# Optimization experiments

Measured on AMD Instinct MI355X. Metric: run time of the kernel, lower is better.

## Reference

```python
import jax, jax.numpy as jnp
import numpy as np

N_NODES = 100000
FEAT_DIM = 128
EMBED_DIM = 128
NUM_SAMPLE = 10


def setup_inputs() -> dict:
    key = jax.random.key(0)
    k1, k2, k3, k4, k5 = jax.random.split(key, 5)
    features = jax.random.normal(k1, (N_NODES, FEAT_DIM), dtype=jnp.float32)
    W1 = jax.random.normal(k2, (EMBED_DIM, FEAT_DIM), dtype=jnp.float32) * (1.0 / np.sqrt(FEAT_DIM))
    W2 = jax.random.normal(k3, (EMBED_DIM, EMBED_DIM), dtype=jnp.float32) * (1.0 / np.sqrt(EMBED_DIM))
    adj = jax.random.randint(k4, (N_NODES, NUM_SAMPLE), 0, N_NODES, dtype=jnp.int64)
    nodes = jax.random.randint(k5, (N_NODES,), 0, N_NODES, dtype=jnp.int64)
    return {"features": features, "W1": W1, "W2": W2, "adj": adj, "nodes": nodes}


def reference(features, W1, W2, adj, nodes):
    # 2-layer GraphSAGE with gcn=True: mean over {self} U sampled neighbors,
    # then relu(agg @ W.T). Layer 1 is computed for all nodes since layer 2
    # needs embeddings of arbitrary neighbors.
    n = features.shape[0]
    self_idx = jnp.arange(n, dtype=adj.dtype)[:, None]            # [N,1]
    neigh1 = jnp.concatenate([self_idx, adj], axis=1)             # [N,S+1]
    agg1 = jnp.mean(features[neigh1], axis=1)                     # [N,F] (gather+mean)
    h1 = jax.nn.relu(agg1 @ W1.T)                                 # [N,E]

    neigh2 = jnp.concatenate([nodes[:, None], adj[nodes]], axis=1)  # [B,S+1]
    agg2 = jnp.mean(h1[neigh2], axis=1)                           # [B,E]
    out = jax.nn.relu(agg2 @ W2.T).T                              # [E,B], Encoder returns embed_dim x num_nodes
    return out
```

## Files before the change

### kernel.cpp

```cpp
#include <hip/hip_runtime.h>

#define N_NODES 100000
#define DIM 128
#define NS 10
#define SCALE (1.0f / 11.0f)
#define NE2 ((size_t)N_NODES * 64)

typedef unsigned int uint;
typedef unsigned short ushort;
typedef __attribute__((ext_vector_type(8))) short bf16x8;
typedef __attribute__((ext_vector_type(4))) float f32x4;

__device__ inline float bl(uint u) {
    union { uint x; float f; } c; c.x = u << 16; return c.f;
}
__device__ inline uint f2b(float x) {
    union { float f; uint u; } c; c.f = x;
    return (c.u + 0x7FFFu + ((c.u >> 16) & 1u)) >> 16;
}

__global__ __launch_bounds__(256) void wsplit(const float* __restrict__ W1,
                                              const float* __restrict__ W2,
                                              ushort* __restrict__ o) {
    const int i = blockIdx.x * 256 + threadIdx.x;
    const float a = W1[i];
    uint h = f2b(a);
    o[i] = (ushort)h;
    o[16384 + i] = (ushort)f2b(a - bl(h));
    const float b = W2[i];
    h = f2b(b);
    o[32768 + i] = (ushort)h;
    o[49152 + i] = (ushort)f2b(b - bl(h));
}

__global__ __launch_bounds__(256, 2) void gemm1(const float* __restrict__ X,
                                                const ushort* __restrict__ Whi,
                                                const ushort* __restrict__ Wlo,
                                                ushort* __restrict__ C) {
    __shared__ __align__(16) ushort lds[8192];
    const int t = threadIdx.x;
    const int lane = t & 63;
    const int wave = t >> 6;
    const int m16 = lane & 15;
    const int kq = lane >> 4;
    const int r0 = blockIdx.x * 32;

    const int v0 = t, v1 = t + 256;
    const int ln0 = v0 & 63, ln1 = v1 & 63;
    const float* s0 = X + (size_t)(r0 + (v0 >> 8) * 16 + (ln0 & 15)) * DIM +
                      ((v0 >> 6) & 3) * 32 + (ln0 >> 4) * 8;
    const float* s1 = X + (size_t)(r0 + (v1 >> 8) * 16 + (ln1 & 15)) * DIM +
                      ((v1 >> 6) & 3) * 32 + (ln1 >> 4) * 8;
    const float4 f00 = *(const float4*)(s0);
    const float4 f01 = *(const float4*)(s0 + 4);
    const float4 f10 = *(const float4*)(s1);
    const float4 f11 = *(const float4*)(s1 + 4);

    bf16x8 wh[2][4], wl[2][4];
#pragma unroll
    for (int c = 0; c < 2; ++c)
#pragma unroll
        for (int ks = 0; ks < 4; ++ks) {
            const size_t off = (size_t)((2 * wave + c) * 16 + m16) * DIM + ks * 32 + kq * 8;
            wh[c][ks] = *(const bf16x8*)(Whi + off);
            wl[c][ks] = *(const bf16x8*)(Wlo + off);
        }

    {
        const float xs[8] = {f00.x, f00.y, f00.z, f00.w, f01.x, f01.y, f01.z, f01.w};
        bf16x8 hi, lo;
#pragma unroll
        for (int j = 0; j < 8; ++j) {
            const uint hb = f2b(xs[j]);
            hi[j] = (short)hb;
            lo[j] = (short)f2b(xs[j] - bl(hb));
        }
        *(bf16x8*)(lds + (v0 >> 6) * 512 + ln0 * 8) = hi;
        *(bf16x8*)(lds + 4096 + (v0 >> 6) * 512 + ln0 * 8) = lo;
    }
    {
        const float xs[8] = {f10.x, f10.y, f10.z, f10.w, f11.x, f11.y, f11.z, f11.w};
        bf16x8 hi, lo;
#pragma unroll
        for (int j = 0; j < 8; ++j) {
            const uint hb = f2b(xs[j]);
            hi[j] = (short)hb;
            lo[j] = (short)f2b(xs[j] - bl(hb));
        }
        *(bf16x8*)(lds + (v1 >> 6) * 512 + ln1 * 8) = hi;
        *(bf16x8*)(lds + 4096 + (v1 >> 6) * 512 + ln1 * 8) = lo;
    }
    __syncthreads();

    f32x4 acc[2][2];
#pragma unroll
    for (int bt = 0; bt < 2; ++bt)
#pragma unroll
        for (int c = 0; c < 2; ++c) acc[bt][c] = (f32x4){0.f, 0.f, 0.f, 0.f};

#pragma unroll
    for (int ks = 0; ks < 4; ++ks) {
#pragma unroll
        for (int bt = 0; bt < 2; ++bt) {
            const int g = bt * 4 + ks;
            const bf16x8 xh = *(const bf16x8*)(lds + g * 512 + lane * 8);
            const bf16x8 xl = *(const bf16x8*)(lds + 4096 + g * 512 + lane * 8);
#pragma unroll
            for (int c = 0; c < 2; ++c) {
                acc[bt][c] = __builtin_amdgcn_mfma_f32_16x16x32_bf16(wh[c][ks], xh, acc[bt][c], 0, 0, 0);
                acc[bt][c] = __builtin_amdgcn_mfma_f32_16x16x32_bf16(wl[c][ks], xh, acc[bt][c], 0, 0, 0);
                acc[bt][c] = __builtin_amdgcn_mfma_f32_16x16x32_bf16(wh[c][ks], xl, acc[bt][c], 0, 0, 0);
            }
        }
    }

#pragma unroll
    for (int bt = 0; bt < 2; ++bt) {
        const size_t row = (size_t)(r0 + bt * 16 + m16);
#pragma unroll
        for (int c = 0; c < 2; ++c) {
            uint2 w;
            w.x = f2b(acc[bt][c][0]) | (f2b(acc[bt][c][1]) << 16);
            w.y = f2b(acc[bt][c][2]) | (f2b(acc[bt][c][3]) << 16);
            *(uint2*)(C + (size_t)(wave >> 1) * NE2 + row * 64 +
                      (2 * (wave & 1) + c) * 16 + kq * 4) = w;
        }
    }
}

__global__ __launch_bounds__(256) void agg1(const ushort* __restrict__ FW,
                                            const int* __restrict__ adj,
                                            ushort* __restrict__ H) {
    __shared__ int idx_lds[320];
    const int t = threadIdx.x;
    const int r0 = blockIdx.x * 32;
    for (int l = t; l < 320; l += 256)
        idx_lds[l] = adj[(size_t)r0 * NS + l];
    __syncthreads();
    const int team = t >> 4;
    const int j = t & 15;
    const int ri0 = team * 2, ri1 = team * 2 + 1;
#pragma unroll
    for (int p = 0; p < 2; ++p) {
        const ushort* FWp = FW + (size_t)p * NE2;
        ushort* Hp = H + (size_t)p * NE2;
        uint2 u0[11], u1[11];
        u0[0] = ((const uint2*)(FWp + (size_t)(r0 + ri0) * 64))[j];
#pragma unroll
        for (int s = 0; s < NS; ++s)
            u0[1 + s] = ((const uint2*)(FWp + (size_t)idx_lds[ri0 * NS + s] * 64))[j];
        u1[0] = ((const uint2*)(FWp + (size_t)(r0 + ri1) * 64))[j];
#pragma unroll
        for (int s = 0; s < NS; ++s)
            u1[1 + s] = ((const uint2*)(FWp + (size_t)idx_lds[ri1 * NS + s] * 64))[j];
        float a0 = 0.f, a1 = 0.f, a2 = 0.f, a3 = 0.f;
        float b0 = 0.f, b1 = 0.f, b2 = 0.f, b3 = 0.f;
#pragma unroll
        for (int s = 0; s < 11; ++s) {
            a0 += bl(u0[s].x); a1 += bl(u0[s].x >> 16);
            a2 += bl(u0[s].y); a3 += bl(u0[s].y >> 16);
            b0 += bl(u1[s].x); b1 += bl(u1[s].x >> 16);
            b2 += bl(u1[s].y); b3 += bl(u1[s].y >> 16);
        }
        uint2 w;
        w.x = f2b(fmaxf(a0 * SCALE, 0.f)) | (f2b(fmaxf(a1 * SCALE, 0.f)) << 16);
        w.y = f2b(fmaxf(a2 * SCALE, 0.f)) | (f2b(fmaxf(a3 * SCALE, 0.f)) << 16);
        ((uint2*)(Hp + (size_t)(r0 + ri0) * 64))[j] = w;
        w.x = f2b(fmaxf(b0 * SCALE, 0.f)) | (f2b(fmaxf(b1 * SCALE, 0.f)) << 16);
        w.y = f2b(fmaxf(b2 * SCALE, 0.f)) | (f2b(fmaxf(b3 * SCALE, 0.f)) << 16);
        ((uint2*)(Hp + (size_t)(r0 + ri1) * 64))[j] = w;
    }
}

__global__ __launch_bounds__(256) void agg2b(const ushort* __restrict__ H,
                                             const int* __restrict__ adj,
                                             const int* __restrict__ nodes,
                                             ushort* __restrict__ P) {
    __shared__ int idx_lds[32 * 11];
    const int t = threadIdx.x;
    const int r0 = blockIdx.x * 32;
    if (t < 32) idx_lds[t * 11] = nodes[r0 + t];
    __syncthreads();
    for (int l = t; l < 320; l += 256) {
        const int bi = l / 10;
        const int s = l - bi * 10;
        idx_lds[bi * 11 + 1 + s] = adj[(size_t)idx_lds[bi * 11] * NS + s];
    }
    __syncthreads();
    const int team = t >> 4;
    const int j = t & 15;
    const int ri0 = team * 2, ri1 = team * 2 + 1;
#pragma unroll
    for (int p = 0; p < 2; ++p) {
        const ushort* Hp = H + (size_t)p * NE2;
        ushort* Pp = P + (size_t)p * NE2;
        uint2 u0[11], u1[11];
#pragma unroll
        for (int s = 0; s < 11; ++s)
            u0[s] = ((const uint2*)(Hp + (size_t)idx_lds[ri0 * 11 + s] * 64))[j];
#pragma unroll
        for (int s = 0; s < 11; ++s)
            u1[s] = ((const uint2*)(Hp + (size_t)idx_lds[ri1 * 11 + s] * 64))[j];
        float a0 = 0.f, a1 = 0.f, a2 = 0.f, a3 = 0.f;
        float b0 = 0.f, b1 = 0.f, b2 = 0.f, b3 = 0.f;
#pragma unroll
        for (int s = 0; s < 11; ++s) {
            a0 += bl(u0[s].x); a1 += bl(u0[s].x >> 16);
            a2 += bl(u0[s].y); a3 += bl(u0[s].y >> 16);
            b0 += bl(u1[s].x); b1 += bl(u1[s].x >> 16);
            b2 += bl(u1[s].y); b3 += bl(u1[s].y >> 16);
        }
        uint2 w;
        w.x = f2b(a0 * SCALE) | (f2b(a1 * SCALE) << 16);
        w.y = f2b(a2 * SCALE) | (f2b(a3 * SCALE) << 16);
        ((uint2*)(Pp + (size_t)(r0 + ri0) * 64))[j] = w;
        w.x = f2b(b0 * SCALE) | (f2b(b1 * SCALE) << 16);
        w.y = f2b(b2 * SCALE) | (f2b(b3 * SCALE) << 16);
        ((uint2*)(Pp + (size_t)(r0 + ri1) * 64))[j] = w;
    }
}

__global__ __launch_bounds__(256, 2) void gemm2t(const ushort* __restrict__ P,
                                                 const ushort* __restrict__ Whi,
                                                 const ushort* __restrict__ Wlo,
                                                 float* __restrict__ out) {
    __shared__ __align__(16) ushort lds[4096];
    const int t = threadIdx.x;
    const int lane = t & 63;
    const int wave = t >> 6;
    const int m16 = lane & 15;
    const int kq = lane >> 4;
    const int r0 = blockIdx.x * 32;

    const int v0 = t, v1 = t + 256;
    const int ln0 = v0 & 63, ln1 = v1 & 63;
    const int ksq0 = (v0 >> 6) & 3, ksq1 = (v1 >> 6) & 3;
    const ushort* s0 = P + (size_t)(ksq0 >> 1) * NE2 +
                       (size_t)(r0 + (v0 >> 8) * 16 + (ln0 & 15)) * 64 +
                       (ksq0 & 1) * 32 + (ln0 >> 4) * 8;
    const ushort* s1 = P + (size_t)(ksq1 >> 1) * NE2 +
                       (size_t)(r0 + (v1 >> 8) * 16 + (ln1 & 15)) * 64 +
                       (ksq1 & 1) * 32 + (ln1 >> 4) * 8;
    const bf16x8 p0 = *(const bf16x8*)(s0);
    const bf16x8 p1 = *(const bf16x8*)(s1);

    bf16x8 wh[2][4], wl[2][4];
#pragma unroll
    for (int c = 0; c < 2; ++c)
#pragma unroll
        for (int ks = 0; ks < 4; ++ks) {
            const size_t off = (size_t)((2 * wave + c) * 16 + m16) * DIM + ks * 32 + kq * 8;
            wh[c][ks] = *(const bf16x8*)(Whi + off);
            wl[c][ks] = *(const bf16x8*)(Wlo + off);
        }

    *(bf16x8*)(lds + (v0 >> 6) * 512 + ln0 * 8) = p0;
    *(bf16x8*)(lds + (v1 >> 6) * 512 + ln1 * 8) = p1;
    __syncthreads();

    f32x4 acc[2][2];
#pragma unroll
    for (int bt = 0; bt < 2; ++bt)
#pragma unroll
        for (int c = 0; c < 2; ++c) acc[bt][c] = (f32x4){0.f, 0.f, 0.f, 0.f};

#pragma unroll
    for (int ks = 0; ks < 4; ++ks) {
#pragma unroll
        for (int bt = 0; bt < 2; ++bt) {
            const bf16x8 pa = *(const bf16x8*)(lds + (bt * 4 + ks) * 512 + lane * 8);
#pragma unroll
            for (int c = 0; c < 2; ++c) {
                acc[bt][c] = __builtin_amdgcn_mfma_f32_16x16x32_bf16(pa, wh[c][ks], acc[bt][c], 0, 0, 0);
                acc[bt][c] = __builtin_amdgcn_mfma_f32_16x16x32_bf16(pa, wl[c][ks], acc[bt][c], 0, 0, 0);
            }
        }
    }

#pragma unroll
    for (int bt = 0; bt < 2; ++bt) {
        const int b = r0 + bt * 16 + kq * 4;
#pragma unroll
        for (int c = 0; c < 2; ++c) {
            const int e = (2 * wave + c) * 16 + m16;
            float4 v;
            v.x = fmaxf(acc[bt][c][0], 0.f);
            v.y = fmaxf(acc[bt][c][1], 0.f);
            v.z = fmaxf(acc[bt][c][2], 0.f);
            v.w = fmaxf(acc[bt][c][3], 0.f);
            *(float4*)(out + (size_t)e * N_NODES + b) = v;
        }
    }
}

extern "C" void kernel_launch(void* const* d_in, const int* in_sizes, int n_in,
                              void* d_out, int out_size, void* d_ws, size_t ws_size,
                              hipStream_t stream) {
    const float* features = (const float*)d_in[0];
    const float* W1 = (const float*)d_in[1];
    const float* W2 = (const float*)d_in[2];
    const int* adj = (const int*)d_in[3];
    const int* nodes = (const int*)d_in[4];
    float* out = (float*)d_out;

    const size_t NE = (size_t)N_NODES * DIM;
    ushort* fw = (ushort*)d_ws;
    ushort* h1 = fw + NE;
    ushort* wpl = h1 + NE;
    ushort* w1hi = wpl;
    ushort* w1lo = wpl + 16384;
    ushort* w2hi = wpl + 32768;
    ushort* w2lo = wpl + 49152;

    wsplit<<<64, 256, 0, stream>>>(W1, W2, wpl);
    gemm1<<<N_NODES / 32, 256, 0, stream>>>(features, w1hi, w1lo, fw);
    agg1<<<N_NODES / 32, 256, 0, stream>>>(fw, adj, h1);
    agg2b<<<N_NODES / 32, 256, 0, stream>>>(h1, adj, nodes, fw);
    gemm2t<<<N_NODES / 32, 256, 0, stream>>>(fw, w2hi, w2lo, out);
}
```

Measured before the change: 154.7 us.

## Fuse layer-2 neighbor aggregation into the layer-2 MFMA GEMM kernel

Merges the agg2b gather-mean kernel and the gemm2t GEMM kernel into one 512-thread kernel. Each thread gathers 11 neighbor rows as 16-byte loads, averages them, and writes the bf16 result straight into LDS in MFMA operand layout. This removes the global round trip of the aggregated matrix and one kernel launch. The cost is larger blocks with more registers per thread, and each wave now handles one 16-column output slice instead of two.

```diff
diff --git a/kernel.cpp b/kernel.cpp
--- a/kernel.cpp
+++ b/kernel.cpp
@@ -172,59 +172,14 @@
     }
 }
 
-__global__ __launch_bounds__(256) void agg2b(const ushort* __restrict__ H,
-                                             const int* __restrict__ adj,
-                                             const int* __restrict__ nodes,
-                                             ushort* __restrict__ P) {
+__global__ __launch_bounds__(512) void gemm2f2(const ushort* __restrict__ H,
+                                               const int* __restrict__ adj,
+                                               const int* __restrict__ nodes,
+                                               const ushort* __restrict__ Whi,
+                                               const ushort* __restrict__ Wlo,
+                                               float* __restrict__ out) {
+    __shared__ __align__(16) ushort plds[4096];
     __shared__ int idx_lds[32 * 11];
-    const int t = threadIdx.x;
-    const int r0 = blockIdx.x * 32;
-    if (t < 32) idx_lds[t * 11] = nodes[r0 + t];
-    __syncthreads();
-    for (int l = t; l < 320; l += 256) {
-        const int bi = l / 10;
-        const int s = l - bi * 10;
-        idx_lds[bi * 11 + 1 + s] = adj[(size_t)idx_lds[bi * 11] * NS + s];
-    }
-    __syncthreads();
-    const int team = t >> 4;
-    const int j = t & 15;
-    const int ri0 = team * 2, ri1 = team * 2 + 1;
-#pragma unroll
-    for (int p = 0; p < 2; ++p) {
-        const ushort* Hp = H + (size_t)p * NE2;
-        ushort* Pp = P + (size_t)p * NE2;
-        uint2 u0[11], u1[11];
-#pragma unroll
-        for (int s = 0; s < 11; ++s)
-            u0[s] = ((const uint2*)(Hp + (size_t)idx_lds[ri0 * 11 + s] * 64))[j];
-#pragma unroll
-        for (int s = 0; s < 11; ++s)
-            u1[s] = ((const uint2*)(Hp + (size_t)idx_lds[ri1 * 11 + s] * 64))[j];
-        float a0 = 0.f, a1 = 0.f, a2 = 0.f, a3 = 0.f;
-        float b0 = 0.f, b1 = 0.f, b2 = 0.f, b3 = 0.f;
-#pragma unroll
-        for (int s = 0; s < 11; ++s) {
-            a0 += bl(u0[s].x); a1 += bl(u0[s].x >> 16);
-            a2 += bl(u0[s].y); a3 += bl(u0[s].y >> 16);
-            b0 += bl(u1[s].x); b1 += bl(u1[s].x >> 16);
-            b2 += bl(u1[s].y); b3 += bl(u1[s].y >> 16);
-        }
-        uint2 w;
-        w.x = f2b(a0 * SCALE) | (f2b(a1 * SCALE) << 16);
-        w.y = f2b(a2 * SCALE) | (f2b(a3 * SCALE) << 16);
-        ((uint2*)(Pp + (size_t)(r0 + ri0) * 64))[j] = w;
-        w.x = f2b(b0 * SCALE) | (f2b(b1 * SCALE) << 16);
-        w.y = f2b(b2 * SCALE) | (f2b(b3 * SCALE) << 16);
-        ((uint2*)(Pp + (size_t)(r0 + ri1) * 64))[j] = w;
-    }
-}
-
-__global__ __launch_bounds__(256, 2) void gemm2t(const ushort* __restrict__ P,
-                                                 const ushort* __restrict__ Whi,
-                                                 const ushort* __restrict__ Wlo,
-                                                 float* __restrict__ out) {
-    __shared__ __align__(16) ushort lds[4096];
     const int t = threadIdx.x;
     const int lane = t & 63;
     const int wave = t >> 6;
@@ -232,64 +187,69 @@
     const int kq = lane >> 4;
     const int r0 = blockIdx.x * 32;
 
-    const int v0 = t, v1 = t + 256;
-    const int ln0 = v0 & 63, ln1 = v1 & 63;
-    const int ksq0 = (v0 >> 6) & 3, ksq1 = (v1 >> 6) & 3;
-    const ushort* s0 = P + (size_t)(ksq0 >> 1) * NE2 +
-                       (size_t)(r0 + (v0 >> 8) * 16 + (ln0 & 15)) * 64 +
-                       (ksq0 & 1) * 32 + (ln0 >> 4) * 8;
-    const ushort* s1 = P + (size_t)(ksq1 >> 1) * NE2 +
-                       (size_t)(r0 + (v1 >> 8) * 16 + (ln1 & 15)) * 64 +
-                       (ksq1 & 1) * 32 + (ln1 >> 4) * 8;
-    const bf16x8 p0 = *(const bf16x8*)(s0);
-    const bf16x8 p1 = *(const bf16x8*)(s1);
-
-    bf16x8 wh[2][4], wl[2][4];
-#pragma unroll
-    for (int c = 0; c < 2; ++c)
-#pragma unroll
-        for (int ks = 0; ks < 4; ++ks) {
-            const size_t off = (size_t)((2 * wave + c) * 16 + m16) * DIM + ks * 32 + kq * 8;
-            wh[c][ks] = *(const bf16x8*)(Whi + off);
-            wl[c][ks] = *(const bf16x8*)(Wlo + off);
-        }
-
-    *(bf16x8*)(lds + (v0 >> 6) * 512 + ln0 * 8) = p0;
-    *(bf16x8*)(lds + (v1 >> 6) * 512 + ln1 * 8) = p1;
-    __syncthreads();
-
-    f32x4 acc[2][2];
-#pragma unroll
-    for (int bt = 0; bt < 2; ++bt)
-#pragma unroll
-        for (int c = 0; c < 2; ++c) acc[bt][c] = (f32x4){0.f, 0.f, 0.f, 0.f};
-
+    bf16x8 wh[4], wl[4];
 #pragma unroll
     for (int ks = 0; ks < 4; ++ks) {
+        const size_t off = (size_t)(wave * 16 + m16) * DIM + ks * 32 + kq * 8;
+        wh[ks] = *(const bf16x8*)(Whi + off);
+        wl[ks] = *(const bf16x8*)(Wlo + off);
+    }
+
+    if (t < 32) idx_lds[t * 11] = nodes[r0 + t];
+    __syncthreads();
+    if (t < 320) {
+        const int bi = t / 10;
+        const int s = t - bi * 10;
+        idx_lds[bi * 11 + 1 + s] = adj[(size_t)idx_lds[bi * 11] * NS + s];
+    }
+    __syncthreads();
+
+    const int ri = (t >> 8) * 16 + (t & 15);
+    const int k0 = ((t >> 6) & 3) * 32 + ((t >> 4) & 3) * 8;
+    const ushort* Hp = H + (size_t)(k0 >> 6) * NE2 + (k0 & 63);
+    uint4 u[11];
+#pragma unroll
+    for (int s = 0; s < 11; ++s)
+        u[s] = *(const uint4*)(Hp + (size_t)idx_lds[ri * 11 + s] * 64);
+    float a[8];
+#pragma unroll
+    for (int k = 0; k < 8; ++k) a[k] = 0.f;
+#pragma unroll
+    for (int s = 0; s < 11; ++s) {
+        a[0] += bl(u[s].x); a[1] += bl(u[s].x >> 16);
+        a[2] += bl(u[s].y); a[3] += bl(u[s].y >> 16);
+        a[4] += bl(u[s].z); a[5] += bl(u[s].z >> 16);
+        a[6] += bl(u[s].w); a[7] += bl(u[s].w >> 16);
+    }
+    bf16x8 pw;
+#pragma unroll
+    for (int k = 0; k < 8; ++k) pw[k] = (short)f2b(a[k] * SCALE);
+    *(bf16x8*)(plds + t * 8) = pw;
+    __syncthreads();
+
+    f32x4 acc[2];
+    acc[0] = (f32x4){0.f, 0.f, 0.f, 0.f};
+    acc[1] = (f32x4){0.f, 0.f, 0.f, 0.f};
+#pragma unroll
+    for (int ks = 0; ks < 4; ++ks) {
 #pragma unroll
         for (int bt = 0; bt < 2; ++bt) {
-            const bf16x8 pa = *(const bf16x8*)(lds + (bt * 4 + ks) * 512 + lane * 8);
-#pragma unroll
-            for (int c = 0; c < 2; ++c) {
-                acc[bt][c] = __builtin_amdgcn_mfma_f32_16x16x32_bf16(pa, wh[c][ks], acc[bt][c], 0, 0, 0);
-                acc[bt][c] = __builtin_amdgcn_mfma_f32_16x16x32_bf16(pa, wl[c][ks], acc[bt][c], 0, 0, 0);
-            }
-        }
-    }
-
+            const bf16x8 pa = *(const bf16x8*)(plds + (bt * 4 + ks) * 512 + lane * 8);
+            acc[bt] = __builtin_amdgcn_mfma_f32_16x16x32_bf16(pa, wh[ks], acc[bt], 0, 0, 0);
+            acc[bt] = __builtin_amdgcn_mfma_f32_16x16x32_bf16(pa, wl[ks], acc[bt], 0, 0, 0);
+        }
+    }
+
+    const int e = wave * 16 + m16;
 #pragma unroll
     for (int bt = 0; bt < 2; ++bt) {
         const int b = r0 + bt * 16 + kq * 4;
-#pragma unroll
-        for (int c = 0; c < 2; ++c) {
-            const int e = (2 * wave + c) * 16 + m16;
-            float4 v;
-            v.x = fmaxf(acc[bt][c][0], 0.f);
-            v.y = fmaxf(acc[bt][c][1], 0.f);
-            v.z = fmaxf(acc[bt][c][2], 0.f);
-            v.w = fmaxf(acc[bt][c][3], 0.f);
-            *(float4*)(out + (size_t)e * N_NODES + b) = v;
-        }
+        float4 v;
+        v.x = fmaxf(acc[bt][0], 0.f);
+        v.y = fmaxf(acc[bt][1], 0.f);
+        v.z = fmaxf(acc[bt][2], 0.f);
+        v.w = fmaxf(acc[bt][3], 0.f);
+        *(float4*)(out + (size_t)e * N_NODES + b) = v;
     }
 }
 
@@ -315,6 +275,5 @@
     wsplit<<<64, 256, 0, stream>>>(W1, W2, wpl);
     gemm1<<<N_NODES / 32, 256, 0, stream>>>(features, w1hi, w1lo, fw);
     agg1<<<N_NODES / 32, 256, 0, stream>>>(fw, adj, h1);
-    agg2b<<<N_NODES / 32, 256, 0, stream>>>(h1, adj, nodes, fw);
-    gemm2t<<<N_NODES / 32, 256, 0, stream>>>(fw, w2hi, w2lo, out);
-}
+    gemm2f2<<<N_NODES / 32, 512, 0, stream>>>(h1, adj, nodes, w2hi, w2lo, out);
+}
```

Measured after the change: 149.7 us. -3.2%, faster.

## Fold weight split into GEMMs and precompute layer-2 neighbor indices in gemm1

Applied to the files above, without the earlier changes.

Removes the separate wsplit launch. Each GEMM block now loads the fp32 weights directly and splits them into bf16 hi/lo pairs in registers. gemm1 also does the dependent nodes->adj index lookup for layer 2 and writes a flat idx2 array, so agg2b just copies contiguous indices instead of chasing pointers. This saves one launch and a serialized dependent load, but every block redoes the weight conversion and gemm1 gains extra scattered reads.

```diff
diff --git a/kernel.cpp b/kernel.cpp
--- a/kernel.cpp
+++ b/kernel.cpp
@@ -5,6 +5,7 @@
 #define NS 10
 #define SCALE (1.0f / 11.0f)
 #define NE2 ((size_t)N_NODES * 64)
+#define NSTRIP 3125
 
 typedef unsigned int uint;
 typedef unsigned short ushort;
@@ -18,25 +19,24 @@
     union { float f; uint u; } c; c.f = x;
     return (c.u + 0x7FFFu + ((c.u >> 16) & 1u)) >> 16;
 }
-
-__global__ __launch_bounds__(256) void wsplit(const float* __restrict__ W1,
-                                              const float* __restrict__ W2,
-                                              ushort* __restrict__ o) {
-    const int i = blockIdx.x * 256 + threadIdx.x;
-    const float a = W1[i];
-    uint h = f2b(a);
-    o[i] = (ushort)h;
-    o[16384 + i] = (ushort)f2b(a - bl(h));
-    const float b = W2[i];
-    h = f2b(b);
-    o[32768 + i] = (ushort)h;
-    o[49152 + i] = (ushort)f2b(b - bl(h));
+__device__ inline void split8(const float* __restrict__ p, bf16x8& h, bf16x8& l) {
+    const float4 a = *(const float4*)p;
+    const float4 b = *(const float4*)(p + 4);
+    const float xs[8] = {a.x, a.y, a.z, a.w, b.x, b.y, b.z, b.w};
+#pragma unroll
+    for (int j = 0; j < 8; ++j) {
+        const uint hb = f2b(xs[j]);
+        h[j] = (short)hb;
+        l[j] = (short)f2b(xs[j] - bl(hb));
+    }
 }
 
 __global__ __launch_bounds__(256, 2) void gemm1(const float* __restrict__ X,
-                                                const ushort* __restrict__ Whi,
-                                                const ushort* __restrict__ Wlo,
-                                                ushort* __restrict__ C) {
+                                                const float* __restrict__ W1,
+                                                const int* __restrict__ adj,
+                                                const int* __restrict__ nodes,
+                                                ushort* __restrict__ C,
+                                                int* __restrict__ idx2) {
     __shared__ __align__(16) ushort lds[8192];
     const int t = threadIdx.x;
     const int lane = t & 63;
@@ -45,50 +45,40 @@
     const int kq = lane >> 4;
     const int r0 = blockIdx.x * 32;
 
+    bf16x8 wh[2][4], wl[2][4];
+#pragma unroll
+    for (int c = 0; c < 2; ++c)
+#pragma unroll
+        for (int ks = 0; ks < 4; ++ks)
+            split8(W1 + (size_t)((2 * wave + c) * 16 + m16) * DIM + ks * 32 + kq * 8,
+                   wh[c][ks], wl[c][ks]);
+
     const int v0 = t, v1 = t + 256;
     const int ln0 = v0 & 63, ln1 = v1 & 63;
-    const float* s0 = X + (size_t)(r0 + (v0 >> 8) * 16 + (ln0 & 15)) * DIM +
-                      ((v0 >> 6) & 3) * 32 + (ln0 >> 4) * 8;
-    const float* s1 = X + (size_t)(r0 + (v1 >> 8) * 16 + (ln1 & 15)) * DIM +
-                      ((v1 >> 6) & 3) * 32 + (ln1 >> 4) * 8;
-    const float4 f00 = *(const float4*)(s0);
-    const float4 f01 = *(const float4*)(s0 + 4);
-    const float4 f10 = *(const float4*)(s1);
-    const float4 f11 = *(const float4*)(s1 + 4);
-
-    bf16x8 wh[2][4], wl[2][4];
-#pragma unroll
-    for (int c = 0; c < 2; ++c)
-#pragma unroll
-        for (int ks = 0; ks < 4; ++ks) {
-            const size_t off = (size_t)((2 * wave + c) * 16 + m16) * DIM + ks * 32 + kq * 8;
-            wh[c][ks] = *(const bf16x8*)(Whi + off);
-            wl[c][ks] = *(const bf16x8*)(Wlo + off);
-        }
-
     {
-        const float xs[8] = {f00.x, f00.y, f00.z, f00.w, f01.x, f01.y, f01.z, f01.w};
+        const float* s0 = X + (size_t)(r0 + (v0 >> 8) * 16 + (ln0 & 15)) * DIM +
+                          ((v0 >> 6) & 3) * 32 + (ln0 >> 4) * 8;
         bf16x8 hi, lo;
-#pragma unroll
-        for (int j = 0; j < 8; ++j) {
-            const uint hb = f2b(xs[j]);
-            hi[j] = (short)hb;
-            lo[j] = (short)f2b(xs[j] - bl(hb));
-        }
+        split8(s0, hi, lo);
         *(bf16x8*)(lds + (v0 >> 6) * 512 + ln0 * 8) = hi;
         *(bf16x8*)(lds + 4096 + (v0 >> 6) * 512 + ln0 * 8) = lo;
     }
     {
-        const float xs[8] = {f10.x, f10.y, f10.z, f10.w, f11.x, f11.y, f11.z, f11.w};
+        const float* s1 = X + (size_t)(r0 + (v1 >> 8) * 16 + (ln1 & 15)) * DIM +
+                          ((v1 >> 6) & 3) * 32 + (ln1 >> 4) * 8;
         bf16x8 hi, lo;
-#pragma unroll
-        for (int j = 0; j < 8; ++j) {
-            const uint hb = f2b(xs[j]);
-            hi[j] = (short)hb;
-            lo[j] = (short)f2b(xs[j] - bl(hb));
-        }
+        split8(s1, hi, lo);
         *(bf16x8*)(lds + (v1 >> 6) * 512 + ln1 * 8) = hi;
         *(bf16x8*)(lds + 4096 + (v1 >> 6) * 512 + ln1 * 8) = lo;
+    }
+
+    if (t < 32) {
+        const int r = r0 + t;
+        const int n = nodes[r];
+        idx2[(size_t)r * 11] = n;
+#pragma unroll
+        for (int s = 0; s < NS; ++s)
+            idx2[(size_t)r * 11 + 1 + s] = adj[(size_t)n * NS + s];
     }
     __syncthreads();
 
@@ -173,19 +163,13 @@
 }
 
 __global__ __launch_bounds__(256) void agg2b(const ushort* __restrict__ H,
-                                             const int* __restrict__ adj,
-                                             const int* __restrict__ nodes,
+                                             const int* __restrict__ idx2,
                                              ushort* __restrict__ P) {
-    __shared__ int idx_lds[32 * 11];
-    const int t = threadIdx.x;
-    const int r0 = blockIdx.x * 32;
-    if (t < 32) idx_lds[t * 11] = nodes[r0 + t];
-    __syncthreads();
-    for (int l = t; l < 320; l += 256) {
-        const int bi = l / 10;
-        const int s = l - bi * 10;
-        idx_lds[bi * 11 + 1 + s] = adj[(size_t)idx_lds[bi * 11] * NS + s];
-    }
+    __shared__ int idx_lds[352];
+    const int t = threadIdx.x;
+    const int r0 = blockIdx.x * 32;
+    for (int l = t; l < 352; l += 256)
+        idx_lds[l] = idx2[(size_t)r0 * 11 + l];
     __syncthreads();
     const int team = t >> 4;
     const int j = t & 15;
@@ -221,8 +205,7 @@
 }
 
 __global__ __launch_bounds__(256, 2) void gemm2t(const ushort* __restrict__ P,
-                                                 const ushort* __restrict__ Whi,
-                                                 const ushort* __restrict__ Wlo,
+                                                 const float* __restrict__ W2,
                                                  float* __restrict__ out) {
     __shared__ __align__(16) ushort lds[4096];
     const int t = threadIdx.x;
@@ -232,30 +215,24 @@
     const int kq = lane >> 4;
     const int r0 = blockIdx.x * 32;
 
-    const int v0 = t, v1 = t + 256;
-    const int ln0 = v0 & 63, ln1 = v1 & 63;
-    const int ksq0 = (v0 >> 6) & 3, ksq1 = (v1 >> 6) & 3;
-    const ushort* s0 = P + (size_t)(ksq0 >> 1) * NE2 +
-                       (size_t)(r0 + (v0 >> 8) * 16 + (ln0 & 15)) * 64 +
-                       (ksq0 & 1) * 32 + (ln0 >> 4) * 8;
-    const ushort* s1 = P + (size_t)(ksq1 >> 1) * NE2 +
-                       (size_t)(r0 + (v1 >> 8) * 16 + (ln1 & 15)) * 64 +
-                       (ksq1 & 1) * 32 + (ln1 >> 4) * 8;
-    const bf16x8 p0 = *(const bf16x8*)(s0);
-    const bf16x8 p1 = *(const bf16x8*)(s1);
+#pragma unroll
+    for (int i = 0; i < 2; ++i) {
+        const int v = t + i * 256;
+        const int ln = v & 63;
+        const int ksq = (v >> 6) & 3;
+        const ushort* s = P + (size_t)(ksq >> 1) * NE2 +
+                          (size_t)(r0 + (v >> 8) * 16 + (ln & 15)) * 64 +
+                          (ksq & 1) * 32 + (ln >> 4) * 8;
+        *(bf16x8*)(lds + (v >> 6) * 512 + ln * 8) = *(const bf16x8*)(s);
+    }
 
     bf16x8 wh[2][4], wl[2][4];
 #pragma unroll
     for (int c = 0; c < 2; ++c)
 #pragma unroll
-        for (int ks = 0; ks < 4; ++ks) {
-            const size_t off = (size_t)((2 * wave + c) * 16 + m16) * DIM + ks * 32 + kq * 8;
-            wh[c][ks] = *(const bf16x8*)(Whi + off);
-            wl[c][ks] = *(const bf16x8*)(Wlo + off);
-        }
-
-    *(bf16x8*)(lds + (v0 >> 6) * 512 + ln0 * 8) = p0;
-    *(bf16x8*)(lds + (v1 >> 6) * 512 + ln1 * 8) = p1;
+        for (int ks = 0; ks < 4; ++ks)
+            split8(W2 + (size_t)((2 * wave + c) * 16 + m16) * DIM + ks * 32 + kq * 8,
+                   wh[c][ks], wl[c][ks]);
     __syncthreads();
 
     f32x4 acc[2][2];
@@ -306,15 +283,10 @@
     const size_t NE = (size_t)N_NODES * DIM;
     ushort* fw = (ushort*)d_ws;
     ushort* h1 = fw + NE;
-    ushort* wpl = h1 + NE;
-    ushort* w1hi = wpl;
-    ushort* w1lo = wpl + 16384;
-    ushort* w2hi = wpl + 32768;
-    ushort* w2lo = wpl + 49152;
-
-    wsplit<<<64, 256, 0, stream>>>(W1, W2, wpl);
-    gemm1<<<N_NODES / 32, 256, 0, stream>>>(features, w1hi, w1lo, fw);
-    agg1<<<N_NODES / 32, 256, 0, stream>>>(fw, adj, h1);
-    agg2b<<<N_NODES / 32, 256, 0, stream>>>(h1, adj, nodes, fw);
-    gemm2t<<<N_NODES / 32, 256, 0, stream>>>(fw, w2hi, w2lo, out);
-}
+    int* idx2 = (int*)(h1 + NE);
+
+    gemm1<<<NSTRIP, 256, 0, stream>>>(features, W1, adj, nodes, fw, idx2);
+    agg1<<<NSTRIP, 256, 0, stream>>>(fw, adj, h1);
+    agg2b<<<NSTRIP, 256, 0, stream>>>(h1, idx2, fw);
+    gemm2t<<<NSTRIP, 256, 0, stream>>>(fw, W2, out);
+}
```

After: 152.6 us. About the same (-1.4%).
